# Kernel optimization log

Measured on AMD Instinct MI355X. Metric: run time of the kernel, lower is better.

## Reference

```python
import jax, jax.numpy as jnp
import numpy as np

EMBED_DIM = 2048
NUM_HEADS = 16
HEAD_DIM = EMBED_DIM // NUM_HEADS  # 128
D_K = 128
SCALE = 1.0 / float(np.sqrt(HEAD_DIM))
LAYER_DEPTH = 6 / 12  # amrpa_layer_idx / n_amrpa_layers
BATCH, SEQ = 2, 2048


def setup_inputs() -> dict:
    key = jax.random.key(0)
    ks = jax.random.split(key, 8)
    return {
        "hidden_states": jax.random.normal(ks[0], (BATCH, SEQ, EMBED_DIM), jnp.float32),
        "c_attn_w": jax.random.normal(ks[1], (EMBED_DIM, 3 * EMBED_DIM), jnp.float32) * 0.02,
        "c_attn_b": jax.random.normal(ks[2], (3 * EMBED_DIM,), jnp.float32) * 0.02,
        "c_proj_w": jax.random.normal(ks[3], (EMBED_DIM, EMBED_DIM), jnp.float32) * 0.02,
        "c_proj_b": jax.random.normal(ks[4], (EMBED_DIM,), jnp.float32) * 0.02,
        "cam_gate": jax.random.normal(ks[5], (D_K,), jnp.float32) * 0.1,
        "cam_w0": jax.random.normal(ks[6], (1,), jnp.float32),
        "cam_w1": jax.random.normal(ks[7], (1,), jnp.float32),
    }


def reference(hidden_states, c_attn_w, c_attn_b, c_proj_w, c_proj_b, cam_gate, cam_w0, cam_w1):
    # GPT2 Conv1D-style fused QKV projection: [B,S,3E]
    qkv = hidden_states @ c_attn_w + c_attn_b
    Q, K, V = jnp.split(qkv, 3, axis=2)  # each [B,S,E]
    # NOTE: faithful to source — attention over the FULL embed dim (no head split),
    # scaled by 1/sqrt(head_dim); causal mask is computed but never applied upstream.
    attn_scores = jnp.einsum('bse,bte->bst', Q, K) * SCALE  # [B,S,S]

    # CAM: sliced low-rank channels
    Q_cam, K_cam, V_cam = Q[:, :, :D_K], K[:, :, :D_K], V[:, :, :D_K]
    # base attention map computed under no_grad in the original
    base_A = jax.lax.stop_gradient(
        jax.nn.softmax(jnp.einsum('bsd,btd->bst', Q_cam, K_cam) * SCALE, axis=-1))
    layer_weight = jax.nn.sigmoid(cam_w0[0] + cam_w1[0] * LAYER_DEPTH)
    cam_ctx = jnp.einsum('bst,btd->bsd', base_A, V_cam)            # [B,S,d_k]
    cam_bias = jnp.einsum('bsd,btd->bst', jnp.tanh(cam_ctx * cam_gate), K_cam)
    cam_bias = cam_bias * (SCALE * layer_weight)                   # cam_mask is all-ones

    final_attn = jax.nn.softmax(attn_scores + cam_bias, axis=-1)
    context = jnp.einsum('bst,bte->bse', final_attn, V)            # [B,S,E]
    output = context @ c_proj_w + c_proj_b                         # resid_dropout is identity (eval)
    return output
```

## Files before the change

kernel.cpp:

```cpp
#include <hip/hip_runtime.h>
#include <hip/hip_bf16.h>

typedef unsigned short u16;
typedef __attribute__((ext_vector_type(8))) __bf16 bf16x8;
typedef __attribute__((ext_vector_type(4))) float f32x4;
typedef __attribute__((ext_vector_type(4))) unsigned short u16x4;

#define SCALE_QK 0.08838834764831845f

__device__ __forceinline__ u16 f2bf(float x) {
  union { float f; unsigned u; } v; v.f = x;
  unsigned r = v.u + 0x7fffu + ((v.u >> 16) & 1u);
  return (u16)(r >> 16);
}

__device__ __forceinline__ void gload_lds16(const u16* g, u16* l) {
  __builtin_amdgcn_global_load_lds(
      (const __attribute__((address_space(1))) unsigned*)g,
      (__attribute__((address_space(3))) unsigned*)l, 16, 0, 0);
}

#define CFENCE() asm volatile("" ::: "memory")

template<bool OUT_BF16, bool HAS_BIAS, bool TWO_SEG>
__global__ __launch_bounds__(512, 2)
void gemm256_8ph(const u16* __restrict__ A1, int lda1, long sA1,
                 const u16* __restrict__ B1, int ldb1, long sB1, int K1,
                 const u16* __restrict__ A2, int lda2, long sA2,
                 const u16* __restrict__ B2, int ldb2, long sB2, int K2,
                 void* __restrict__ Cv, int ldc, long sC,
                 float scale, const float* __restrict__ bias, int nbx)
{
  extern __shared__ u16 lds[];
  const int bz = blockIdx.z;

  const int nwg = gridDim.x;
  const int orig = blockIdx.x;
  const int q8 = nwg >> 3, r8 = nwg & 7;
  const int xcd = orig & 7, lp = orig >> 3;
  const int wg = (xcd < r8 ? xcd * (q8 + 1) : r8 * (q8 + 1) + (xcd - r8) * q8) + lp;
  const int bx = wg % nbx, by = wg / nbx;
  const long m0 = (long)by * 256, n0 = (long)bx * 256;

  const int tid = threadIdx.x;
  const int wid = tid >> 6, lane = tid & 63;
  const int wm = wid >> 2, wn = wid & 3;
  const int rl = lane & 15, g = lane >> 4;
  const int swk = ((g ^ ((rl >> 1) & 3)) << 3);

  int aoff[8], boff[4];
#pragma unroll
  for (int i = 0; i < 8; ++i)
    aoff[i] = (wm * 128 + i * 16 + rl) * 32 + swk;
#pragma unroll
  for (int j = 0; j < 4; ++j)
    boff[j] = 16384 + (wn * 64 + j * 16 + rl) * 32 + swk;

  const int Rl = tid >> 2;
  const int scol = (((tid & 3) ^ ((tid >> 3) & 3)) << 3);
  const int sdst = wid * 512;

  f32x4 acc[8][4];
#pragma unroll
  for (int i = 0; i < 8; ++i)
#pragma unroll
    for (int j = 0; j < 4; ++j) acc[i][j] = (f32x4){0.f, 0.f, 0.f, 0.f};

#define STAGE_A(KK, KB, BQ)                                                  \
  gload_lds16(rA0 + (KB) + (KK) * 32, (BQ) + (KK) * 8192 + sdst);            \
  gload_lds16(rA1 + (KB) + (KK) * 32, (BQ) + (KK) * 8192 + 4096 + sdst);
#define STAGE_B(KK, KB, BQ)                                                  \
  gload_lds16(rB0 + (KB) + (KK) * 32, (BQ) + 16384 + (KK) * 8192 + sdst);    \
  gload_lds16(rB1 + (KB) + (KK) * 32, (BQ) + 16384 + (KK) * 8192 + 4096 + sdst);
#define PHASE_MFMA(IH)                                                       \
  __builtin_amdgcn_s_setprio(1);                                             \
  _Pragma("unroll")                                                          \
  for (int i = 0; i < 4; ++i)                                                \
    _Pragma("unroll")                                                        \
    for (int j = 0; j < 4; ++j)                                              \
      acc[(IH) * 4 + i][j] = __builtin_amdgcn_mfma_f32_16x16x32_bf16(        \
          av[i], bv[j], acc[(IH) * 4 + i][j], 0, 0, 0);                      \
  __builtin_amdgcn_s_setprio(0);

  const int NSEG = TWO_SEG ? 2 : 1;
#pragma unroll 1
  for (int seg = 0; seg < NSEG; ++seg) {
    const u16* Ap = (seg == 0) ? (A1 + (long)bz * sA1) : (A2 + (long)bz * sA2);
    const u16* Bp = (seg == 0) ? (B1 + (long)bz * sB1) : (B2 + (long)bz * sB2);
    const int lda = (seg == 0) ? lda1 : lda2;
    const int ldb = (seg == 0) ? ldb1 : ldb2;
    const int K   = (seg == 0) ? K1 : K2;
    const int NT  = K >> 6;

    const u16* rA0 = Ap + (m0 + Rl) * (long)lda + scol;
    const u16* rA1 = Ap + (m0 + Rl + 128) * (long)lda + scol;
    const u16* rB0 = Bp + (n0 + Rl) * (long)ldb + scol;
    const u16* rB1 = Bp + (n0 + Rl + 128) * (long)ldb + scol;

    __builtin_amdgcn_s_barrier();
    CFENCE();
    STAGE_A(0, 0, lds);
    STAGE_B(0, 0, lds);
    STAGE_A(1, 0, lds);
    STAGE_B(1, 0, lds);
    CFENCE();

#pragma unroll 1
    for (int t = 0; t < NT; ++t) {
      const u16* bp = lds + (t & 1) * 32768;
      u16* bq = lds + ((t + 1) & 1) * 32768;
      const bool hn = (t + 1) < NT;
      const int kn = (t + 1) << 6;

      bf16x8 av[4], bv[4];

      asm volatile("s_waitcnt vmcnt(4)" ::: "memory");
      __builtin_amdgcn_s_barrier();
      CFENCE();
      if (hn) { STAGE_A(0, kn, bq); }
#pragma unroll
      for (int i = 0; i < 4; ++i) av[i] = *(const bf16x8*)(bp + aoff[i]);
#pragma unroll
      for (int j = 0; j < 4; ++j) bv[j] = *(const bf16x8*)(bp + boff[j]);
      PHASE_MFMA(0)
      CFENCE();

      if (hn) { STAGE_B(0, kn, bq); }
#pragma unroll
      for (int i = 0; i < 4; ++i) av[i] = *(const bf16x8*)(bp + aoff[4 + i]);
      PHASE_MFMA(1)
      CFENCE();

      if (hn) { asm volatile("s_waitcnt vmcnt(4)" ::: "memory"); }
      else    { asm volatile("s_waitcnt vmcnt(0)" ::: "memory"); }
      __builtin_amdgcn_s_barrier();
      CFENCE();
      if (hn) { STAGE_A(1, kn, bq); }
#pragma unroll
      for (int i = 0; i < 4; ++i) av[i] = *(const bf16x8*)(bp + 8192 + aoff[i]);
#pragma unroll
      for (int j = 0; j < 4; ++j) bv[j] = *(const bf16x8*)(bp + 8192 + boff[j]);
      PHASE_MFMA(0)
      CFENCE();

      if (hn) { STAGE_B(1, kn, bq); }
#pragma unroll
      for (int i = 0; i < 4; ++i) av[i] = *(const bf16x8*)(bp + 8192 + aoff[4 + i]);
      PHASE_MFMA(1)
      CFENCE();
    }
  }
#undef STAGE_A
#undef STAGE_B
#undef PHASE_MFMA

  const int r0 = (lane >> 4) << 2;
  const int cL = lane & 15;
#pragma unroll
  for (int i = 0; i < 8; ++i) {
#pragma unroll
    for (int j = 0; j < 4; ++j) {
      const long row = m0 + wm * 128 + i * 16 + r0;
      const long col = n0 + wn * 64 + j * 16 + cL;
      float bvs = 0.f;
      if (HAS_BIAS) bvs = bias[col];
      if (OUT_BF16) {
        u16* Cp = (u16*)Cv + (long)bz * sC;
#pragma unroll
        for (int r = 0; r < 4; ++r)
          Cp[(row + r) * ldc + col] = f2bf(acc[i][j][r] * scale + bvs);
      } else {
        float* Cp = (float*)Cv + (long)bz * sC;
#pragma unroll
        for (int r = 0; r < 4; ++r)
          Cp[(row + r) * ldc + col] = acc[i][j][r] * scale + bvs;
      }
    }
  }
}

template<bool OUT_BF16, bool HAS_BIAS>
__global__ __launch_bounds__(256)
void gemm_bt(const u16* __restrict__ A, int lda, long sA,
             const u16* __restrict__ B, int ldb, long sB,
             void* __restrict__ Cv, int ldc, long sC,
             int K, float scale, const float* __restrict__ bias)
{
  __shared__ u16 As[128 * 64];
  __shared__ u16 Bs[128 * 64];
  const int bz   = blockIdx.z;
  const u16* Ap  = A + (long)bz * sA;
  const u16* Bp  = B + (long)bz * sB;
  const int tid  = threadIdx.x;
  const int wid  = tid >> 6;
  const int lane = tid & 63;
  const long m0  = (long)blockIdx.y * 128;
  const long n0  = (long)blockIdx.x * 128;
  const int lrow = lane >> 3;
  const int lk   = (lane & 7) << 3;
  const int wr   = wid >> 1, wc = wid & 1;

  f32x4 acc[4][4];
#pragma unroll
  for (int i = 0; i < 4; ++i)
#pragma unroll
    for (int j = 0; j < 4; ++j) acc[i][j] = (f32x4){0.f, 0.f, 0.f, 0.f};

  for (int k0 = 0; k0 < K; k0 += 64) {
#pragma unroll
    for (int c4 = 0; c4 < 4; ++c4) {
      const int chunk = (wid << 2) + c4;
      gload_lds16(Ap + (m0 + (chunk << 3) + lrow) * lda + k0 + lk, &As[chunk << 9]);
      gload_lds16(Bp + (n0 + (chunk << 3) + lrow) * ldb + k0 + lk, &Bs[chunk << 9]);
    }
    __syncthreads();
#pragma unroll
    for (int kk = 0; kk < 2; ++kk) {
      bf16x8 af[4], bfr[4];
      const int kof   = (kk << 5) + ((lane >> 4) << 3);
      const int rbase = lane & 15;
#pragma unroll
      for (int i = 0; i < 4; ++i)
        af[i] = *(const bf16x8*)&As[(((wr << 6) + (i << 4) + rbase) << 6) + kof];
#pragma unroll
      for (int j = 0; j < 4; ++j)
        bfr[j] = *(const bf16x8*)&Bs[(((wc << 6) + (j << 4) + rbase) << 6) + kof];
#pragma unroll
      for (int i = 0; i < 4; ++i)
#pragma unroll
        for (int j = 0; j < 4; ++j)
          acc[i][j] = __builtin_amdgcn_mfma_f32_16x16x32_bf16(af[i], bfr[j], acc[i][j], 0, 0, 0);
    }
    __syncthreads();
  }

  const int r0 = (lane >> 4) << 2;
  const int cL = lane & 15;
#pragma unroll
  for (int i = 0; i < 4; ++i) {
#pragma unroll
    for (int j = 0; j < 4; ++j) {
      const long row = m0 + (wr << 6) + (i << 4) + r0;
      const long col = n0 + (wc << 6) + (j << 4) + cL;
      float bv = 0.f;
      if (HAS_BIAS) bv = bias[col];
      if (OUT_BF16) {
        u16* Cp = (u16*)Cv + (long)bz * sC;
#pragma unroll
        for (int r = 0; r < 4; ++r)
          Cp[(row + r) * ldc + col] = f2bf(acc[i][j][r] * scale + bv);
      } else {
        float* Cp = (float*)Cv + (long)bz * sC;
#pragma unroll
        for (int r = 0; r < 4; ++r)
          Cp[(row + r) * ldc + col] = acc[i][j][r] * scale + bv;
      }
    }
  }
}

__global__ __launch_bounds__(256)
void gemm_bt_splitk(const u16* __restrict__ A, int lda, long sA,
                    const u16* __restrict__ B, int ldb, long sB,
                    float* __restrict__ C, int ldc, long sC,
                    int Kslice, float scale)
{
  __shared__ u16 As[128 * 64];
  __shared__ u16 Bs[128 * 64];
  const int ks = blockIdx.z & 7;
  const int bz = blockIdx.z >> 3;
  const u16* Ap  = A + (long)bz * sA + ks * Kslice;
  const u16* Bp  = B + (long)bz * sB + ks * Kslice;
  const int tid  = threadIdx.x;
  const int wid  = tid >> 6;
  const int lane = tid & 63;
  const long m0  = (long)blockIdx.y * 128;
  const long n0  = (long)blockIdx.x * 128;
  const int lrow = lane >> 3;
  const int lk   = (lane & 7) << 3;
  const int wr   = wid >> 1, wc = wid & 1;

  f32x4 acc[4][4];
#pragma unroll
  for (int i = 0; i < 4; ++i)
#pragma unroll
    for (int j = 0; j < 4; ++j) acc[i][j] = (f32x4){0.f, 0.f, 0.f, 0.f};

  for (int k0 = 0; k0 < Kslice; k0 += 64) {
#pragma unroll
    for (int c4 = 0; c4 < 4; ++c4) {
      const int chunk = (wid << 2) + c4;
      gload_lds16(Ap + (m0 + (chunk << 3) + lrow) * lda + k0 + lk, &As[chunk << 9]);
      gload_lds16(Bp + (n0 + (chunk << 3) + lrow) * ldb + k0 + lk, &Bs[chunk << 9]);
    }
    __syncthreads();
#pragma unroll
    for (int kk = 0; kk < 2; ++kk) {
      bf16x8 af[4], bfr[4];
      const int kof   = (kk << 5) + ((lane >> 4) << 3);
      const int rbase = lane & 15;
#pragma unroll
      for (int i = 0; i < 4; ++i)
        af[i] = *(const bf16x8*)&As[(((wr << 6) + (i << 4) + rbase) << 6) + kof];
#pragma unroll
      for (int j = 0; j < 4; ++j)
        bfr[j] = *(const bf16x8*)&Bs[(((wc << 6) + (j << 4) + rbase) << 6) + kof];
#pragma unroll
      for (int i = 0; i < 4; ++i)
#pragma unroll
        for (int j = 0; j < 4; ++j)
          acc[i][j] = __builtin_amdgcn_mfma_f32_16x16x32_bf16(af[i], bfr[j], acc[i][j], 0, 0, 0);
    }
    __syncthreads();
  }

  const int r0 = (lane >> 4) << 2;
  const int cL = lane & 15;
  float* Cp = C + (long)bz * sC;
#pragma unroll
  for (int i = 0; i < 4; ++i) {
#pragma unroll
    for (int j = 0; j < 4; ++j) {
      const long row = m0 + (wr << 6) + (i << 4) + r0;
      const long col = n0 + (wc << 6) + (j << 4) + cL;
#pragma unroll
      for (int r = 0; r < 4; ++r)
        atomicAdd(&Cp[(row + r) * ldc + col], acc[i][j][r] * scale);
    }
  }
}

__global__ __launch_bounds__(256)
void softmax_rows2048(const float* __restrict__ src, u16* __restrict__ dst) {
  const long row = blockIdx.x;
  const float4* s = (const float4*)(src + row * 2048);
  const int tid = threadIdx.x;
  float4 a = s[tid * 2], b = s[tid * 2 + 1];
  float m = fmaxf(fmaxf(fmaxf(a.x, a.y), fmaxf(a.z, a.w)),
                  fmaxf(fmaxf(b.x, b.y), fmaxf(b.z, b.w)));
#pragma unroll
  for (int o = 32; o > 0; o >>= 1) m = fmaxf(m, __shfl_xor(m, o));
  __shared__ float redm[4];
  __shared__ float reds[4];
  if ((tid & 63) == 0) redm[tid >> 6] = m;
  __syncthreads();
  m = fmaxf(fmaxf(redm[0], redm[1]), fmaxf(redm[2], redm[3]));
  float e[8];
  e[0] = __expf(a.x - m); e[1] = __expf(a.y - m); e[2] = __expf(a.z - m); e[3] = __expf(a.w - m);
  e[4] = __expf(b.x - m); e[5] = __expf(b.y - m); e[6] = __expf(b.z - m); e[7] = __expf(b.w - m);
  float sum = e[0] + e[1] + e[2] + e[3] + e[4] + e[5] + e[6] + e[7];
#pragma unroll
  for (int o = 32; o > 0; o >>= 1) sum += __shfl_xor(sum, o);
  if ((tid & 63) == 0) reds[tid >> 6] = sum;
  __syncthreads();
  sum = reds[0] + reds[1] + reds[2] + reds[3];
  const float inv = 1.f / sum;
  u16x4 o1 = { f2bf(e[0] * inv), f2bf(e[1] * inv), f2bf(e[2] * inv), f2bf(e[3] * inv) };
  u16x4 o2 = { f2bf(e[4] * inv), f2bf(e[5] * inv), f2bf(e[6] * inv), f2bf(e[7] * inv) };
  u16x4* d = (u16x4*)(dst + row * 2048);
  d[tid * 2]     = o1;
  d[tid * 2 + 1] = o2;
}

__global__ void transpose_f32_to_bf16(const float* __restrict__ src, u16* __restrict__ dst,
                                      int R, int C) {
  __shared__ float t[32][33];
  const int c0 = blockIdx.x * 32, r0 = blockIdx.y * 32;
  const int tx = threadIdx.x, ty = threadIdx.y;
#pragma unroll
  for (int i = 0; i < 4; ++i)
    t[ty + i * 8][tx] = src[(long)(r0 + ty + i * 8) * C + c0 + tx];
  __syncthreads();
#pragma unroll
  for (int i = 0; i < 4; ++i)
    dst[(long)(c0 + ty + i * 8) * R + r0 + tx] = f2bf(t[tx][ty + i * 8]);
}

__global__ void transpose_bf16_batched(const u16* __restrict__ src, int ss, long sbat,
                                       u16* __restrict__ dst, int ds, long dbat) {
  __shared__ u16 t[32][33];
  const u16* s = src + (long)blockIdx.z * sbat;
  u16* d = dst + (long)blockIdx.z * dbat;
  const int c0 = blockIdx.x * 32, r0 = blockIdx.y * 32;
  const int tx = threadIdx.x, ty = threadIdx.y;
#pragma unroll
  for (int i = 0; i < 4; ++i)
    t[ty + i * 8][tx] = s[(long)(r0 + ty + i * 8) * ss + c0 + tx];
  __syncthreads();
#pragma unroll
  for (int i = 0; i < 4; ++i)
    d[(long)(c0 + ty + i * 8) * ds + r0 + tx] = t[tx][ty + i * 8];
}

__global__ __launch_bounds__(256)
void convert_f32_to_bf16(const float* __restrict__ src, u16* __restrict__ dst, long n4) {
  long i = (long)blockIdx.x * 256 + threadIdx.x;
  if (i < n4) {
    float4 v = ((const float4*)src)[i];
    *(u16x4*)(dst + i * 4) = (u16x4){ f2bf(v.x), f2bf(v.y), f2bf(v.z), f2bf(v.w) };
  }
}

__global__ __launch_bounds__(256)
void cam_tanh_kernel(const float* __restrict__ ctx, const float* __restrict__ gate,
                     const float* __restrict__ lw, u16* __restrict__ out, int n) {
  int i = blockIdx.x * 256 + threadIdx.x;
  if (i < n) {
    int d = i & 127;
    out[i] = f2bf(tanhf(ctx[i] * gate[d]) * lw[0]);
  }
}

__global__ __launch_bounds__(256)
void zero_f32(float* __restrict__ p, int n) {
  int i = blockIdx.x * 256 + threadIdx.x;
  if (i < n) p[i] = 0.f;
}

__global__ void calc_lw_kernel(const float* w0, const float* w1, float* lw) {
  *lw = 1.f / (1.f + __expf(-(w0[0] + 0.5f * w1[0])));
}

extern "C" void kernel_launch(void* const* d_in, const int* in_sizes, int n_in,
                              void* d_out, int out_size, void* d_ws, size_t ws_size,
                              hipStream_t stream) {
  const float* hs       = (const float*)d_in[0];
  const float* c_attn_w = (const float*)d_in[1];
  const float* c_attn_b = (const float*)d_in[2];
  const float* c_proj_w = (const float*)d_in[3];
  const float* c_proj_b = (const float*)d_in[4];
  const float* cam_gate = (const float*)d_in[5];
  const float* cam_w0   = (const float*)d_in[6];
  const float* cam_w1   = (const float*)d_in[7];
  float* out = (float*)d_out;

  char* w = (char*)d_ws;
  float* lw      = (float*)(w + 0);
  u16*   hs_b    = (u16*)(w + 256);
  u16*   waT_b   = (u16*)(w + 256 + 16777216UL);
  u16*   wpT_b   = (u16*)(w + 256 + 41943040UL);
  u16*   qkv_b   = (u16*)(w + 256 + 50331648UL);
  u16*   vT_b    = (u16*)(w + 256 + 100663296UL);
  float* scoresF = (float*)(w + 256 + 117440512UL);
  float* camS    = (float*)(w + 256 + 150994944UL);
  float* ctxF    = (float*)(w + 256 + 184549376UL);
  u16*   camT_b  = (u16*)(w + 256 + 186646528UL);
  u16* baseA_b = hs_b;
  u16* P_b     = (u16*)camS;
  u16* ctxE_b  = (u16*)scoresF;

  dim3 b256(256);

  hipFuncSetAttribute((const void*)gemm256_8ph<true,  true,  false>,
                      hipFuncAttributeMaxDynamicSharedMemorySize, 131072);
  hipFuncSetAttribute((const void*)gemm256_8ph<false, false, true>,
                      hipFuncAttributeMaxDynamicSharedMemorySize, 131072);
  hipFuncSetAttribute((const void*)gemm256_8ph<true,  false, false>,
                      hipFuncAttributeMaxDynamicSharedMemorySize, 131072);
  hipFuncSetAttribute((const void*)gemm256_8ph<false, true,  false>,
                      hipFuncAttributeMaxDynamicSharedMemorySize, 131072);

  calc_lw_kernel<<<dim3(1), dim3(1), 0, stream>>>(cam_w0, cam_w1, lw);
  convert_f32_to_bf16<<<dim3(8192), b256, 0, stream>>>(hs, hs_b, 2097152L);
  transpose_f32_to_bf16<<<dim3(192, 64), dim3(32, 8), 0, stream>>>(c_attn_w, waT_b, 2048, 6144);
  transpose_f32_to_bf16<<<dim3(64, 64), dim3(32, 8), 0, stream>>>(c_proj_w, wpT_b, 2048, 2048);

  gemm256_8ph<true, true, false><<<dim3(384, 1, 1), dim3(512), 131072, stream>>>(
      hs_b, 2048, 0L, waT_b, 2048, 0L, 2048,
      nullptr, 0, 0L, nullptr, 0, 0L, 0,
      qkv_b, 6144, 0L, 1.f, c_attn_b, 24);

  transpose_bf16_batched<<<dim3(64, 64, 2), dim3(32, 8), 0, stream>>>(
      qkv_b + 4096, 6144, 2048L * 6144, vT_b, 2048, 2048L * 2048);

  gemm_bt<false, false><<<dim3(16, 16, 2), b256, 0, stream>>>(
      qkv_b, 6144, 2048L * 6144, qkv_b + 2048, 6144, 2048L * 6144,
      camS, 2048, 2048L * 2048, 128, SCALE_QK, nullptr);

  softmax_rows2048<<<dim3(4096), b256, 0, stream>>>(camS, baseA_b);

  zero_f32<<<dim3(2048), b256, 0, stream>>>(ctxF, 524288);
  gemm_bt_splitk<<<dim3(1, 16, 16), b256, 0, stream>>>(
      baseA_b, 2048, 2048L * 2048, vT_b, 2048, 2048L * 2048,
      ctxF, 128, 2048L * 128, 256, 1.f);

  cam_tanh_kernel<<<dim3(2048), b256, 0, stream>>>(ctxF, cam_gate, lw, camT_b, 524288);

  gemm256_8ph<false, false, true><<<dim3(64, 1, 2), dim3(512), 131072, stream>>>(
      qkv_b, 6144, 2048L * 6144, qkv_b + 2048, 6144, 2048L * 6144, 2048,
      camT_b, 128, 2048L * 128, qkv_b + 2048, 6144, 2048L * 6144, 128,
      scoresF, 2048, 2048L * 2048, SCALE_QK, nullptr, 8);

  softmax_rows2048<<<dim3(4096), b256, 0, stream>>>(scoresF, P_b);

  gemm256_8ph<true, false, false><<<dim3(64, 1, 2), dim3(512), 131072, stream>>>(
      P_b, 2048, 2048L * 2048, vT_b, 2048, 2048L * 2048, 2048,
      nullptr, 0, 0L, nullptr, 0, 0L, 0,
      ctxE_b, 2048, 2048L * 2048, 1.f, nullptr, 8);

  gemm256_8ph<false, true, false><<<dim3(128, 1, 1), dim3(512), 131072, stream>>>(
      ctxE_b, 2048, 0L, wpT_b, 2048, 0L, 2048,
      nullptr, 0, 0L, nullptr, 0, 0L, 0,
      out, 2048, 0L, 1.f, c_proj_b, 8);
}
```

Before: 392.4 us.

## Deepen GEMM LDS pipeline to 4 stages and add 256x128 tile variant

The 256x256 GEMM is rebuilt around a 4-slot LDS ring of 32-wide K halves. It keeps three stages in flight, with explicit vmcnt waits and sched barriers around the MFMA phases instead of the old double buffer. A new 256x128 tile kernel with the same deeper prefetch replaces the 256x256 kernel for the score, PV and output-projection GEMMs. This doubles their grid sizes so more of the GPU's compute units are filled. The cost is more B-operand reloads per output and more barriers per K step.

```diff
diff --git a/kernel.cpp b/kernel.cpp
--- a/kernel.cpp
+++ b/kernel.cpp
@@ -21,146 +21,234 @@
 }
 
 #define CFENCE() asm volatile("" ::: "memory")
-
-template<bool OUT_BF16, bool HAS_BIAS, bool TWO_SEG>
+#define WAITV(N) asm volatile("s_waitcnt vmcnt(" #N ")" ::: "memory")
+
+#define MM_PROLOG()                                                      \
+  CFENCE(); __builtin_amdgcn_s_barrier();                                \
+  asm volatile("s_waitcnt lgkmcnt(0)" ::: "memory");                     \
+  __builtin_amdgcn_sched_barrier(0);                                     \
+  __builtin_amdgcn_s_setprio(1);
+#define MM_EPILOG()                                                      \
+  __builtin_amdgcn_s_setprio(0);                                         \
+  CFENCE(); __builtin_amdgcn_s_barrier(); CFENCE();
+
+template<bool OUT_BF16, bool HAS_BIAS>
 __global__ __launch_bounds__(512, 2)
-void gemm256_8ph(const u16* __restrict__ A1, int lda1, long sA1,
-                 const u16* __restrict__ B1, int ldb1, long sB1, int K1,
-                 const u16* __restrict__ A2, int lda2, long sA2,
-                 const u16* __restrict__ B2, int ldb2, long sB2, int K2,
-                 void* __restrict__ Cv, int ldc, long sC,
-                 float scale, const float* __restrict__ bias, int nbx)
+void g256(const u16* __restrict__ A, int lda, long sA,
+          const u16* __restrict__ B, int ldb, long sB,
+          void* __restrict__ Cv, int ldc, long sC,
+          int K, float scale, const float* __restrict__ bias, int nbx)
 {
   extern __shared__ u16 lds[];
   const int bz = blockIdx.z;
-
-  const int nwg = gridDim.x;
-  const int orig = blockIdx.x;
+  const int nwg = gridDim.x, orig = blockIdx.x;
   const int q8 = nwg >> 3, r8 = nwg & 7;
   const int xcd = orig & 7, lp = orig >> 3;
   const int wg = (xcd < r8 ? xcd * (q8 + 1) : r8 * (q8 + 1) + (xcd - r8) * q8) + lp;
   const int bx = wg % nbx, by = wg / nbx;
   const long m0 = (long)by * 256, n0 = (long)bx * 256;
 
-  const int tid = threadIdx.x;
-  const int wid = tid >> 6, lane = tid & 63;
+  const int tid = threadIdx.x, wid = tid >> 6, lane = tid & 63;
   const int wm = wid >> 2, wn = wid & 3;
   const int rl = lane & 15, g = lane >> 4;
-  const int swk = ((g ^ ((rl >> 1) & 3)) << 3);
+  const int sw = ((g ^ ((rl >> 1) & 3)) << 3);
 
   int aoff[8], boff[4];
 #pragma unroll
+  for (int i = 0; i < 8; ++i) aoff[i] = (wm * 128 + i * 16 + rl) * 32 + sw;
+#pragma unroll
+  for (int j = 0; j < 4; ++j) boff[j] = (wn * 64 + j * 16 + rl) * 32 + sw;
+
+  const u16* Ab = A + (long)bz * sA + m0 * lda;
+  const u16* Bb = B + (long)bz * sB + n0 * ldb;
+  const int srow = tid >> 2;
+  const int scolX = (((tid & 3) ^ ((srow >> 1) & 3)) << 3);
+
+#define ST_A(H_) {                                                       \
+    const u16* s_ = Ab + (long)srow * lda + (H_) * 32 + scolX;           \
+    u16* d_ = lds + (((H_) & 3) * 8192) + tid * 8;                       \
+    gload_lds16(s_, d_); gload_lds16(s_ + (long)128 * lda, d_ + 4096); }
+#define ST_B(H_) {                                                       \
+    const u16* s_ = Bb + (long)srow * ldb + (H_) * 32 + scolX;           \
+    u16* d_ = lds + 32768 + (((H_) & 3) * 8192) + tid * 8;               \
+    gload_lds16(s_, d_); gload_lds16(s_ + (long)128 * ldb, d_ + 4096); }
+#define RDA(H_, IH) { const u16* aS_ = lds + ((H_) & 3) * 8192;          \
+    _Pragma("unroll") for (int i = 0; i < 4; ++i)                        \
+      av[i] = *(const bf16x8*)(aS_ + aoff[(IH) * 4 + i]); }
+#define RDB(H_) { const u16* bS_ = lds + 32768 + ((H_) & 3) * 8192;      \
+    _Pragma("unroll") for (int j = 0; j < 4; ++j)                        \
+      bv[j] = *(const bf16x8*)(bS_ + boff[j]); }
+#define MFMA16(IH)                                                       \
+  MM_PROLOG();                                                           \
+  _Pragma("unroll") for (int i = 0; i < 4; ++i)                          \
+    _Pragma("unroll") for (int j = 0; j < 4; ++j)                        \
+      acc[(IH) * 4 + i][j] = __builtin_amdgcn_mfma_f32_16x16x32_bf16(    \
+          av[i], bv[j], acc[(IH) * 4 + i][j], 0, 0, 0);                  \
+  MM_EPILOG();
+
+  f32x4 acc[8][4];
+#pragma unroll
   for (int i = 0; i < 8; ++i)
-    aoff[i] = (wm * 128 + i * 16 + rl) * 32 + swk;
-#pragma unroll
-  for (int j = 0; j < 4; ++j)
-    boff[j] = 16384 + (wn * 64 + j * 16 + rl) * 32 + swk;
-
-  const int Rl = tid >> 2;
-  const int scol = (((tid & 3) ^ ((tid >> 3) & 3)) << 3);
-  const int sdst = wid * 512;
-
-  f32x4 acc[8][4];
-#pragma unroll
-  for (int i = 0; i < 8; ++i)
 #pragma unroll
     for (int j = 0; j < 4; ++j) acc[i][j] = (f32x4){0.f, 0.f, 0.f, 0.f};
 
-#define STAGE_A(KK, KB, BQ)                                                  \
-  gload_lds16(rA0 + (KB) + (KK) * 32, (BQ) + (KK) * 8192 + sdst);            \
-  gload_lds16(rA1 + (KB) + (KK) * 32, (BQ) + (KK) * 8192 + 4096 + sdst);
-#define STAGE_B(KK, KB, BQ)                                                  \
-  gload_lds16(rB0 + (KB) + (KK) * 32, (BQ) + 16384 + (KK) * 8192 + sdst);    \
-  gload_lds16(rB1 + (KB) + (KK) * 32, (BQ) + 16384 + (KK) * 8192 + 4096 + sdst);
-#define PHASE_MFMA(IH)                                                       \
-  __builtin_amdgcn_s_setprio(1);                                             \
-  _Pragma("unroll")                                                          \
-  for (int i = 0; i < 4; ++i)                                                \
-    _Pragma("unroll")                                                        \
-    for (int j = 0; j < 4; ++j)                                              \
-      acc[(IH) * 4 + i][j] = __builtin_amdgcn_mfma_f32_16x16x32_bf16(        \
-          av[i], bv[j], acc[(IH) * 4 + i][j], 0, 0, 0);                      \
-  __builtin_amdgcn_s_setprio(0);
+  const int NT = K >> 6;
+
+  ST_A(0); ST_B(0); ST_A(1); ST_B(1); ST_A(2); ST_B(2);
+  WAITV(8);
+  CFENCE(); __builtin_amdgcn_s_barrier(); CFENCE();
+
+#pragma unroll 1
+  for (int t = 0; t < NT - 2; ++t) {
+    const int h0 = 2 * t, h1 = 2 * t + 1;
+    bf16x8 av[4], bv[4];
+    RDA(h0, 0); RDB(h0); ST_A(h1 + 2); MFMA16(0);
+    RDA(h0, 1); ST_B(h1 + 2); WAITV(8); MFMA16(1);
+    RDA(h1, 0); RDB(h1); ST_A(h1 + 3); MFMA16(0);
+    RDA(h1, 1); ST_B(h1 + 3); WAITV(8); MFMA16(1);
+  }
+  {
+    const int h0 = 2 * NT - 4, h1 = 2 * NT - 3;
+    bf16x8 av[4], bv[4];
+    RDA(h0, 0); RDB(h0); ST_A(2 * NT - 1); MFMA16(0);
+    RDA(h0, 1); ST_B(2 * NT - 1); WAITV(8); MFMA16(1);
+    RDA(h1, 0); RDB(h1); MFMA16(0);
+    RDA(h1, 1); WAITV(4); MFMA16(1);
+  }
+  {
+    const int h0 = 2 * NT - 2, h1 = 2 * NT - 1;
+    bf16x8 av[4], bv[4];
+    RDA(h0, 0); RDB(h0); MFMA16(0);
+    RDA(h0, 1); WAITV(0); MFMA16(1);
+    RDA(h1, 0); RDB(h1); MFMA16(0);
+    RDA(h1, 1); MFMA16(1);
+  }
+#undef ST_A
+#undef ST_B
+#undef RDA
+#undef RDB
+#undef MFMA16
+
+  const int r0 = (lane >> 4) << 2;
+  const int cL = lane & 15;
+#pragma unroll
+  for (int i = 0; i < 8; ++i) {
+#pragma unroll
+    for (int j = 0; j < 4; ++j) {
+      const long row = m0 + wm * 128 + i * 16 + r0;
+      const long col = n0 + wn * 64 + j * 16 + cL;
+      float bvs = 0.f;
+      if (HAS_BIAS) bvs = bias[col];
+      if (OUT_BF16) {
+        u16* Cp = (u16*)Cv + (long)bz * sC;
+#pragma unroll
+        for (int r = 0; r < 4; ++r)
+          Cp[(row + r) * ldc + col] = f2bf(acc[i][j][r] * scale + bvs);
+      } else {
+        float* Cp = (float*)Cv + (long)bz * sC;
+#pragma unroll
+        for (int r = 0; r < 4; ++r)
+          Cp[(row + r) * ldc + col] = acc[i][j][r] * scale + bvs;
+      }
+    }
+  }
+}
+
+template<bool OUT_BF16, bool HAS_BIAS, bool TWO_SEG>
+__global__ __launch_bounds__(512, 2)
+void g128(const u16* __restrict__ A1, int lda1, long sA1,
+          const u16* __restrict__ B1, int ldb1, long sB1, int K1,
+          const u16* __restrict__ A2, int lda2, long sA2,
+          const u16* __restrict__ B2, int ldb2, long sB2, int K2,
+          void* __restrict__ Cv, int ldc, long sC,
+          float scale, const float* __restrict__ bias, int nbx)
+{
+  extern __shared__ u16 lds[];
+  const int bz = blockIdx.z;
+  const int nwg = gridDim.x, orig = blockIdx.x;
+  const int q8 = nwg >> 3, r8 = nwg & 7;
+  const int xcd = orig & 7, lp = orig >> 3;
+  const int wg = (xcd < r8 ? xcd * (q8 + 1) : r8 * (q8 + 1) + (xcd - r8) * q8) + lp;
+  const int bx = wg % nbx, by = wg / nbx;
+  const long m0 = (long)by * 256, n0 = (long)bx * 128;
+
+  const int tid = threadIdx.x, wid = tid >> 6, lane = tid & 63;
+  const int wm = wid >> 1, wn = wid & 1;
+  const int rl = lane & 15, g = lane >> 4;
+  const int sw = ((g ^ ((rl >> 1) & 3)) << 3);
+
+  int aoff[4], boff[4];
+#pragma unroll
+  for (int i = 0; i < 4; ++i) aoff[i] = (wm * 64 + i * 16 + rl) * 32 + sw;
+#pragma unroll
+  for (int j = 0; j < 4; ++j) boff[j] = (wn * 64 + j * 16 + rl) * 32 + sw;
+
+  const int srow = tid >> 2;
+  const int scolX = (((tid & 3) ^ ((srow >> 1) & 3)) << 3);
+
+  f32x4 acc[4][4];
+#pragma unroll
+  for (int i = 0; i < 4; ++i)
+#pragma unroll
+    for (int j = 0; j < 4; ++j) acc[i][j] = (f32x4){0.f, 0.f, 0.f, 0.f};
+
+#define STG128(H_) {                                                     \
+    const u16* sa_ = Ab + (long)srow * lda + (H_) * 32 + scolX;          \
+    u16* da_ = lds + (((H_) & 3) * 8192) + tid * 8;                      \
+    gload_lds16(sa_, da_); gload_lds16(sa_ + (long)128 * lda, da_ + 4096); \
+    gload_lds16(Bb + (long)srow * ldb + (H_) * 32 + scolX,               \
+                lds + 32768 + (((H_) & 3) * 4096) + tid * 8); }
+#define RD128(H_) {                                                      \
+    const u16* aS_ = lds + ((H_) & 3) * 8192;                            \
+    const u16* bS_ = lds + 32768 + ((H_) & 3) * 4096;                    \
+    _Pragma("unroll") for (int i = 0; i < 4; ++i)                        \
+      av[i] = *(const bf16x8*)(aS_ + aoff[i]);                           \
+    _Pragma("unroll") for (int j = 0; j < 4; ++j)                        \
+      bv[j] = *(const bf16x8*)(bS_ + boff[j]); }
+#define MM128()                                                          \
+  MM_PROLOG();                                                           \
+  _Pragma("unroll") for (int i = 0; i < 4; ++i)                          \
+    _Pragma("unroll") for (int j = 0; j < 4; ++j)                        \
+      acc[i][j] = __builtin_amdgcn_mfma_f32_16x16x32_bf16(               \
+          av[i], bv[j], acc[i][j], 0, 0, 0);                             \
+  MM_EPILOG();
 
   const int NSEG = TWO_SEG ? 2 : 1;
 #pragma unroll 1
   for (int seg = 0; seg < NSEG; ++seg) {
-    const u16* Ap = (seg == 0) ? (A1 + (long)bz * sA1) : (A2 + (long)bz * sA2);
-    const u16* Bp = (seg == 0) ? (B1 + (long)bz * sB1) : (B2 + (long)bz * sB2);
+    const u16* Ab = ((seg == 0) ? A1 + (long)bz * sA1 : A2 + (long)bz * sA2);
+    const u16* Bb = ((seg == 0) ? B1 + (long)bz * sB1 : B2 + (long)bz * sB2);
     const int lda = (seg == 0) ? lda1 : lda2;
     const int ldb = (seg == 0) ? ldb1 : ldb2;
     const int K   = (seg == 0) ? K1 : K2;
-    const int NT  = K >> 6;
-
-    const u16* rA0 = Ap + (m0 + Rl) * (long)lda + scol;
-    const u16* rA1 = Ap + (m0 + Rl + 128) * (long)lda + scol;
-    const u16* rB0 = Bp + (n0 + Rl) * (long)ldb + scol;
-    const u16* rB1 = Bp + (n0 + Rl + 128) * (long)ldb + scol;
-
-    __builtin_amdgcn_s_barrier();
-    CFENCE();
-    STAGE_A(0, 0, lds);
-    STAGE_B(0, 0, lds);
-    STAGE_A(1, 0, lds);
-    STAGE_B(1, 0, lds);
-    CFENCE();
+    Ab += m0 * lda;
+    Bb += n0 * ldb;
+    const int H = K >> 5;
+
+    bf16x8 av[4], bv[4];
+    STG128(0); STG128(1); STG128(2);
+    WAITV(6);
+    CFENCE(); __builtin_amdgcn_s_barrier(); CFENCE();
 
 #pragma unroll 1
-    for (int t = 0; t < NT; ++t) {
-      const u16* bp = lds + (t & 1) * 32768;
-      u16* bq = lds + ((t + 1) & 1) * 32768;
-      const bool hn = (t + 1) < NT;
-      const int kn = (t + 1) << 6;
-
-      bf16x8 av[4], bv[4];
-
-      asm volatile("s_waitcnt vmcnt(4)" ::: "memory");
-      __builtin_amdgcn_s_barrier();
-      CFENCE();
-      if (hn) { STAGE_A(0, kn, bq); }
-#pragma unroll
-      for (int i = 0; i < 4; ++i) av[i] = *(const bf16x8*)(bp + aoff[i]);
-#pragma unroll
-      for (int j = 0; j < 4; ++j) bv[j] = *(const bf16x8*)(bp + boff[j]);
-      PHASE_MFMA(0)
-      CFENCE();
-
-      if (hn) { STAGE_B(0, kn, bq); }
-#pragma unroll
-      for (int i = 0; i < 4; ++i) av[i] = *(const bf16x8*)(bp + aoff[4 + i]);
-      PHASE_MFMA(1)
-      CFENCE();
-
-      if (hn) { asm volatile("s_waitcnt vmcnt(4)" ::: "memory"); }
-      else    { asm volatile("s_waitcnt vmcnt(0)" ::: "memory"); }
-      __builtin_amdgcn_s_barrier();
-      CFENCE();
-      if (hn) { STAGE_A(1, kn, bq); }
-#pragma unroll
-      for (int i = 0; i < 4; ++i) av[i] = *(const bf16x8*)(bp + 8192 + aoff[i]);
-#pragma unroll
-      for (int j = 0; j < 4; ++j) bv[j] = *(const bf16x8*)(bp + 8192 + boff[j]);
-      PHASE_MFMA(0)
-      CFENCE();
-
-      if (hn) { STAGE_B(1, kn, bq); }
-#pragma unroll
-      for (int i = 0; i < 4; ++i) av[i] = *(const bf16x8*)(bp + 8192 + aoff[4 + i]);
-      PHASE_MFMA(1)
-      CFENCE();
-    }
-  }
-#undef STAGE_A
-#undef STAGE_B
-#undef PHASE_MFMA
+    for (int h = 0; h < H - 3; ++h) {
+      RD128(h); STG128(h + 3); WAITV(6); MM128();
+    }
+    RD128(H - 3); WAITV(3); MM128();
+    RD128(H - 2); WAITV(0); MM128();
+    RD128(H - 1); MM128();
+  }
+#undef STG128
+#undef RD128
+#undef MM128
 
   const int r0 = (lane >> 4) << 2;
   const int cL = lane & 15;
 #pragma unroll
-  for (int i = 0; i < 8; ++i) {
+  for (int i = 0; i < 4; ++i) {
 #pragma unroll
     for (int j = 0; j < 4; ++j) {
-      const long row = m0 + wm * 128 + i * 16 + r0;
+      const long row = m0 + wm * 64 + i * 16 + r0;
       const long col = n0 + wn * 64 + j * 16 + cL;
       float bvs = 0.f;
       if (HAS_BIAS) bvs = bias[col];
@@ -451,24 +539,23 @@
 
   dim3 b256(256);
 
-  hipFuncSetAttribute((const void*)gemm256_8ph<true,  true,  false>,
+  hipFuncSetAttribute((const void*)g256<true, true>,
                       hipFuncAttributeMaxDynamicSharedMemorySize, 131072);
-  hipFuncSetAttribute((const void*)gemm256_8ph<false, false, true>,
-                      hipFuncAttributeMaxDynamicSharedMemorySize, 131072);
-  hipFuncSetAttribute((const void*)gemm256_8ph<true,  false, false>,
-                      hipFuncAttributeMaxDynamicSharedMemorySize, 131072);
-  hipFuncSetAttribute((const void*)gemm256_8ph<false, true,  false>,
-                      hipFuncAttributeMaxDynamicSharedMemorySize, 131072);
+  hipFuncSetAttribute((const void*)g128<false, false, true>,
+                      hipFuncAttributeMaxDynamicSharedMemorySize, 98304);
+  hipFuncSetAttribute((const void*)g128<true, false, false>,
+                      hipFuncAttributeMaxDynamicSharedMemorySize, 98304);
+  hipFuncSetAttribute((const void*)g128<false, true, false>,
+                      hipFuncAttributeMaxDynamicSharedMemorySize, 98304);
 
   calc_lw_kernel<<<dim3(1), dim3(1), 0, stream>>>(cam_w0, cam_w1, lw);
   convert_f32_to_bf16<<<dim3(8192), b256, 0, stream>>>(hs, hs_b, 2097152L);
   transpose_f32_to_bf16<<<dim3(192, 64), dim3(32, 8), 0, stream>>>(c_attn_w, waT_b, 2048, 6144);
   transpose_f32_to_bf16<<<dim3(64, 64), dim3(32, 8), 0, stream>>>(c_proj_w, wpT_b, 2048, 2048);
 
-  gemm256_8ph<true, true, false><<<dim3(384, 1, 1), dim3(512), 131072, stream>>>(
-      hs_b, 2048, 0L, waT_b, 2048, 0L, 2048,
-      nullptr, 0, 0L, nullptr, 0, 0L, 0,
-      qkv_b, 6144, 0L, 1.f, c_attn_b, 24);
+  g256<true, true><<<dim3(384, 1, 1), dim3(512), 131072, stream>>>(
+      hs_b, 2048, 0L, waT_b, 2048, 0L,
+      qkv_b, 6144, 0L, 2048, 1.f, c_attn_b, 24);
 
   transpose_bf16_batched<<<dim3(64, 64, 2), dim3(32, 8), 0, stream>>>(
       qkv_b + 4096, 6144, 2048L * 6144, vT_b, 2048, 2048L * 2048);
@@ -486,20 +573,20 @@
 
   cam_tanh_kernel<<<dim3(2048), b256, 0, stream>>>(ctxF, cam_gate, lw, camT_b, 524288);
 
-  gemm256_8ph<false, false, true><<<dim3(64, 1, 2), dim3(512), 131072, stream>>>(
+  g128<false, false, true><<<dim3(128, 1, 2), dim3(512), 98304, stream>>>(
       qkv_b, 6144, 2048L * 6144, qkv_b + 2048, 6144, 2048L * 6144, 2048,
       camT_b, 128, 2048L * 128, qkv_b + 2048, 6144, 2048L * 6144, 128,
-      scoresF, 2048, 2048L * 2048, SCALE_QK, nullptr, 8);
+      scoresF, 2048, 2048L * 2048, SCALE_QK, nullptr, 16);
 
   softmax_rows2048<<<dim3(4096), b256, 0, stream>>>(scoresF, P_b);
 
-  gemm256_8ph<true, false, false><<<dim3(64, 1, 2), dim3(512), 131072, stream>>>(
+  g128<true, false, false><<<dim3(128, 1, 2), dim3(512), 98304, stream>>>(
       P_b, 2048, 2048L * 2048, vT_b, 2048, 2048L * 2048, 2048,
       nullptr, 0, 0L, nullptr, 0, 0L, 0,
-      ctxE_b, 2048, 2048L * 2048, 1.f, nullptr, 8);
-
-  gemm256_8ph<false, true, false><<<dim3(128, 1, 1), dim3(512), 131072, stream>>>(
+      ctxE_b, 2048, 2048L * 2048, 1.f, nullptr, 16);
+
+  g128<false, true, false><<<dim3(256, 1, 1), dim3(512), 98304, stream>>>(
       ctxE_b, 2048, 0L, wpT_b, 2048, 0L, 2048,
       nullptr, 0, 0L, nullptr, 0, 0L, 0,
-      out, 2048, 0L, 1.f, c_proj_b, 8);
-}
+      out, 2048, 0L, 1.f, c_proj_b, 16);
+}
```

Result: faster. 349.9 us (median of 2 runs) (-10.8%).

## Replace 256x256 GEMM with 256x128 tile and 4-stage LDS pipeline

Applied to the files above, without the earlier changes.

The main GEMM kernel changes from 256x256 output tiles with a two-buffer, K=64 schedule to 256x128 tiles with a four-stage ring of K=32 LDS slices. Register fragments are double-buffered so the LDS reads for the next slice are issued after the current MFMAs. Grids double to keep the same coverage, and LDS per block drops to 96KB. This aims to put more workgroups on the GPU and hide more global-load latency, at the cost of lower arithmetic intensity per tile and more redundant global traffic.

```diff
diff --git a/kernel.cpp b/kernel.cpp
--- a/kernel.cpp
+++ b/kernel.cpp
@@ -21,146 +21,116 @@
 }
 
 #define CFENCE() asm volatile("" ::: "memory")
+#define WAITV(N) asm volatile("s_waitcnt vmcnt(" #N ")" ::: "memory")
 
 template<bool OUT_BF16, bool HAS_BIAS, bool TWO_SEG>
 __global__ __launch_bounds__(512, 2)
-void gemm256_8ph(const u16* __restrict__ A1, int lda1, long sA1,
-                 const u16* __restrict__ B1, int ldb1, long sB1, int K1,
-                 const u16* __restrict__ A2, int lda2, long sA2,
-                 const u16* __restrict__ B2, int ldb2, long sB2, int K2,
-                 void* __restrict__ Cv, int ldc, long sC,
-                 float scale, const float* __restrict__ bias, int nbx)
+void g128p(const u16* __restrict__ A1, int lda1, long sA1,
+           const u16* __restrict__ B1, int ldb1, long sB1, int K1,
+           const u16* __restrict__ A2, int lda2, long sA2,
+           const u16* __restrict__ B2, int ldb2, long sB2, int K2,
+           void* __restrict__ Cv, int ldc, long sC,
+           float scale, const float* __restrict__ bias, int nbx)
 {
   extern __shared__ u16 lds[];
   const int bz = blockIdx.z;
-
-  const int nwg = gridDim.x;
-  const int orig = blockIdx.x;
+  const int nwg = gridDim.x, orig = blockIdx.x;
   const int q8 = nwg >> 3, r8 = nwg & 7;
   const int xcd = orig & 7, lp = orig >> 3;
   const int wg = (xcd < r8 ? xcd * (q8 + 1) : r8 * (q8 + 1) + (xcd - r8) * q8) + lp;
   const int bx = wg % nbx, by = wg / nbx;
-  const long m0 = (long)by * 256, n0 = (long)bx * 256;
-
-  const int tid = threadIdx.x;
-  const int wid = tid >> 6, lane = tid & 63;
-  const int wm = wid >> 2, wn = wid & 3;
+  const long m0 = (long)by * 256, n0 = (long)bx * 128;
+
+  const int tid = threadIdx.x, wid = tid >> 6, lane = tid & 63;
+  const int wm = wid >> 1, wn = wid & 1;
   const int rl = lane & 15, g = lane >> 4;
-  const int swk = ((g ^ ((rl >> 1) & 3)) << 3);
-
-  int aoff[8], boff[4];
-#pragma unroll
-  for (int i = 0; i < 8; ++i)
-    aoff[i] = (wm * 128 + i * 16 + rl) * 32 + swk;
-#pragma unroll
-  for (int j = 0; j < 4; ++j)
-    boff[j] = 16384 + (wn * 64 + j * 16 + rl) * 32 + swk;
-
-  const int Rl = tid >> 2;
-  const int scol = (((tid & 3) ^ ((tid >> 3) & 3)) << 3);
-  const int sdst = wid * 512;
-
-  f32x4 acc[8][4];
-#pragma unroll
-  for (int i = 0; i < 8; ++i)
+  const int sw = ((g ^ ((rl >> 1) & 3)) << 3);
+
+  int aoff[4], boff[4];
+#pragma unroll
+  for (int i = 0; i < 4; ++i) aoff[i] = (wm * 64 + i * 16 + rl) * 32 + sw;
+#pragma unroll
+  for (int j = 0; j < 4; ++j) boff[j] = (wn * 64 + j * 16 + rl) * 32 + sw;
+
+  const int srow = tid >> 2;
+  const int scolX = (((tid & 3) ^ ((srow >> 1) & 3)) << 3);
+
+  f32x4 acc[4][4];
+#pragma unroll
+  for (int i = 0; i < 4; ++i)
 #pragma unroll
     for (int j = 0; j < 4; ++j) acc[i][j] = (f32x4){0.f, 0.f, 0.f, 0.f};
 
-#define STAGE_A(KK, KB, BQ)                                                  \
-  gload_lds16(rA0 + (KB) + (KK) * 32, (BQ) + (KK) * 8192 + sdst);            \
-  gload_lds16(rA1 + (KB) + (KK) * 32, (BQ) + (KK) * 8192 + 4096 + sdst);
-#define STAGE_B(KK, KB, BQ)                                                  \
-  gload_lds16(rB0 + (KB) + (KK) * 32, (BQ) + 16384 + (KK) * 8192 + sdst);    \
-  gload_lds16(rB1 + (KB) + (KK) * 32, (BQ) + 16384 + (KK) * 8192 + 4096 + sdst);
-#define PHASE_MFMA(IH)                                                       \
-  __builtin_amdgcn_s_setprio(1);                                             \
-  _Pragma("unroll")                                                          \
-  for (int i = 0; i < 4; ++i)                                                \
-    _Pragma("unroll")                                                        \
-    for (int j = 0; j < 4; ++j)                                              \
-      acc[(IH) * 4 + i][j] = __builtin_amdgcn_mfma_f32_16x16x32_bf16(        \
-          av[i], bv[j], acc[(IH) * 4 + i][j], 0, 0, 0);                      \
-  __builtin_amdgcn_s_setprio(0);
+  bf16x8 avA[4], bvA[4], avB[4], bvB[4];
+
+#define STG(H_) {                                                        \
+    const int h_ = (H_);                                                 \
+    const u16* sa_ = Ab + (long)srow * lda + h_ * 32 + scolX;            \
+    u16* da_ = lds + ((h_ & 3) * 8192) + tid * 8;                        \
+    gload_lds16(sa_, da_);                                               \
+    gload_lds16(sa_ + (long)128 * lda, da_ + 4096);                      \
+    gload_lds16(Bb + (long)srow * ldb + h_ * 32 + scolX,                 \
+                lds + 32768 + ((h_ & 3) * 4096) + tid * 8); }
+#define RD(H_, AV, BV) {                                                 \
+    const u16* aS_ = lds + (((H_) & 3) * 8192);                          \
+    const u16* bS_ = lds + 32768 + (((H_) & 3) * 4096);                  \
+    _Pragma("unroll") for (int i_ = 0; i_ < 4; ++i_)                     \
+      AV[i_] = *(const bf16x8*)(aS_ + aoff[i_]);                         \
+    _Pragma("unroll") for (int j_ = 0; j_ < 4; ++j_)                     \
+      BV[j_] = *(const bf16x8*)(bS_ + boff[j_]); }
+#define BODY(K_, CAV, CBV, NAV, NBV, W_STMT, DO_RD, DO_ST)               \
+    W_STMT;                                                              \
+    CFENCE(); __builtin_amdgcn_s_barrier(); CFENCE();                    \
+    asm volatile("s_waitcnt lgkmcnt(0)" ::: "memory");                   \
+    __builtin_amdgcn_sched_barrier(0);                                   \
+    __builtin_amdgcn_s_setprio(1);                                       \
+    _Pragma("unroll") for (int i_ = 0; i_ < 4; ++i_)                     \
+      _Pragma("unroll") for (int j_ = 0; j_ < 4; ++j_)                   \
+        acc[i_][j_] = __builtin_amdgcn_mfma_f32_16x16x32_bf16(           \
+            CAV[i_], CBV[j_], acc[i_][j_], 0, 0, 0);                     \
+    __builtin_amdgcn_s_setprio(0);                                       \
+    if (DO_RD) { RD((K_) + 1, NAV, NBV); }                               \
+    if (DO_ST) { STG((K_) + 4); }                                        \
+    CFENCE();
 
   const int NSEG = TWO_SEG ? 2 : 1;
 #pragma unroll 1
   for (int seg = 0; seg < NSEG; ++seg) {
-    const u16* Ap = (seg == 0) ? (A1 + (long)bz * sA1) : (A2 + (long)bz * sA2);
-    const u16* Bp = (seg == 0) ? (B1 + (long)bz * sB1) : (B2 + (long)bz * sB2);
     const int lda = (seg == 0) ? lda1 : lda2;
     const int ldb = (seg == 0) ? ldb1 : ldb2;
     const int K   = (seg == 0) ? K1 : K2;
-    const int NT  = K >> 6;
-
-    const u16* rA0 = Ap + (m0 + Rl) * (long)lda + scol;
-    const u16* rA1 = Ap + (m0 + Rl + 128) * (long)lda + scol;
-    const u16* rB0 = Bp + (n0 + Rl) * (long)ldb + scol;
-    const u16* rB1 = Bp + (n0 + Rl + 128) * (long)ldb + scol;
-
-    __builtin_amdgcn_s_barrier();
+    const u16* Ab = ((seg == 0) ? A1 + (long)bz * sA1 : A2 + (long)bz * sA2) + m0 * (long)lda;
+    const u16* Bb = ((seg == 0) ? B1 + (long)bz * sB1 : B2 + (long)bz * sB2) + n0 * (long)ldb;
+    const int H = K >> 5;
+
+    STG(0); STG(1); STG(2);
+    WAITV(6);
+    CFENCE(); __builtin_amdgcn_s_barrier(); CFENCE();
+    RD(0, avA, bvA);
+    STG(3);
     CFENCE();
-    STAGE_A(0, 0, lds);
-    STAGE_B(0, 0, lds);
-    STAGE_A(1, 0, lds);
-    STAGE_B(1, 0, lds);
-    CFENCE();
 
 #pragma unroll 1
-    for (int t = 0; t < NT; ++t) {
-      const u16* bp = lds + (t & 1) * 32768;
-      u16* bq = lds + ((t + 1) & 1) * 32768;
-      const bool hn = (t + 1) < NT;
-      const int kn = (t + 1) << 6;
-
-      bf16x8 av[4], bv[4];
-
-      asm volatile("s_waitcnt vmcnt(4)" ::: "memory");
-      __builtin_amdgcn_s_barrier();
-      CFENCE();
-      if (hn) { STAGE_A(0, kn, bq); }
-#pragma unroll
-      for (int i = 0; i < 4; ++i) av[i] = *(const bf16x8*)(bp + aoff[i]);
-#pragma unroll
-      for (int j = 0; j < 4; ++j) bv[j] = *(const bf16x8*)(bp + boff[j]);
-      PHASE_MFMA(0)
-      CFENCE();
-
-      if (hn) { STAGE_B(0, kn, bq); }
-#pragma unroll
-      for (int i = 0; i < 4; ++i) av[i] = *(const bf16x8*)(bp + aoff[4 + i]);
-      PHASE_MFMA(1)
-      CFENCE();
-
-      if (hn) { asm volatile("s_waitcnt vmcnt(4)" ::: "memory"); }
-      else    { asm volatile("s_waitcnt vmcnt(0)" ::: "memory"); }
-      __builtin_amdgcn_s_barrier();
-      CFENCE();
-      if (hn) { STAGE_A(1, kn, bq); }
-#pragma unroll
-      for (int i = 0; i < 4; ++i) av[i] = *(const bf16x8*)(bp + 8192 + aoff[i]);
-#pragma unroll
-      for (int j = 0; j < 4; ++j) bv[j] = *(const bf16x8*)(bp + 8192 + boff[j]);
-      PHASE_MFMA(0)
-      CFENCE();
-
-      if (hn) { STAGE_B(1, kn, bq); }
-#pragma unroll
-      for (int i = 0; i < 4; ++i) av[i] = *(const bf16x8*)(bp + 8192 + aoff[4 + i]);
-      PHASE_MFMA(1)
-      CFENCE();
-    }
-  }
-#undef STAGE_A
-#undef STAGE_B
-#undef PHASE_MFMA
+    for (int k = 0; k + 5 < H; k += 2) {
+      BODY(k,     avA, bvA, avB, bvB, WAITV(6), true, true);
+      BODY(k + 1, avB, bvB, avA, bvA, WAITV(6), true, true);
+    }
+    BODY(H - 4, avA, bvA, avB, bvB, WAITV(6), true,  false);
+    BODY(H - 3, avB, bvB, avA, bvA, WAITV(3), true,  false);
+    BODY(H - 2, avA, bvA, avB, bvB, WAITV(0), true,  false);
+    BODY(H - 1, avB, bvB, avA, bvA, (void)0,  false, false);
+  }
+#undef STG
+#undef RD
+#undef BODY
 
   const int r0 = (lane >> 4) << 2;
   const int cL = lane & 15;
 #pragma unroll
-  for (int i = 0; i < 8; ++i) {
+  for (int i = 0; i < 4; ++i) {
 #pragma unroll
     for (int j = 0; j < 4; ++j) {
-      const long row = m0 + wm * 128 + i * 16 + r0;
+      const long row = m0 + wm * 64 + i * 16 + r0;
       const long col = n0 + wn * 64 + j * 16 + cL;
       float bvs = 0.f;
       if (HAS_BIAS) bvs = bias[col];
@@ -451,24 +421,24 @@
 
   dim3 b256(256);
 
-  hipFuncSetAttribute((const void*)gemm256_8ph<true,  true,  false>,
-                      hipFuncAttributeMaxDynamicSharedMemorySize, 131072);
-  hipFuncSetAttribute((const void*)gemm256_8ph<false, false, true>,
-                      hipFuncAttributeMaxDynamicSharedMemorySize, 131072);
-  hipFuncSetAttribute((const void*)gemm256_8ph<true,  false, false>,
-                      hipFuncAttributeMaxDynamicSharedMemorySize, 131072);
-  hipFuncSetAttribute((const void*)gemm256_8ph<false, true,  false>,
-                      hipFuncAttributeMaxDynamicSharedMemorySize, 131072);
+  hipFuncSetAttribute((const void*)g128p<true, true, false>,
+                      hipFuncAttributeMaxDynamicSharedMemorySize, 98304);
+  hipFuncSetAttribute((const void*)g128p<false, false, true>,
+                      hipFuncAttributeMaxDynamicSharedMemorySize, 98304);
+  hipFuncSetAttribute((const void*)g128p<true, false, false>,
+                      hipFuncAttributeMaxDynamicSharedMemorySize, 98304);
+  hipFuncSetAttribute((const void*)g128p<false, true, false>,
+                      hipFuncAttributeMaxDynamicSharedMemorySize, 98304);
 
   calc_lw_kernel<<<dim3(1), dim3(1), 0, stream>>>(cam_w0, cam_w1, lw);
   convert_f32_to_bf16<<<dim3(8192), b256, 0, stream>>>(hs, hs_b, 2097152L);
   transpose_f32_to_bf16<<<dim3(192, 64), dim3(32, 8), 0, stream>>>(c_attn_w, waT_b, 2048, 6144);
   transpose_f32_to_bf16<<<dim3(64, 64), dim3(32, 8), 0, stream>>>(c_proj_w, wpT_b, 2048, 2048);
 
-  gemm256_8ph<true, true, false><<<dim3(384, 1, 1), dim3(512), 131072, stream>>>(
+  g128p<true, true, false><<<dim3(768, 1, 1), dim3(512), 98304, stream>>>(
       hs_b, 2048, 0L, waT_b, 2048, 0L, 2048,
       nullptr, 0, 0L, nullptr, 0, 0L, 0,
-      qkv_b, 6144, 0L, 1.f, c_attn_b, 24);
+      qkv_b, 6144, 0L, 1.f, c_attn_b, 48);
 
   transpose_bf16_batched<<<dim3(64, 64, 2), dim3(32, 8), 0, stream>>>(
       qkv_b + 4096, 6144, 2048L * 6144, vT_b, 2048, 2048L * 2048);
@@ -486,20 +456,20 @@
 
   cam_tanh_kernel<<<dim3(2048), b256, 0, stream>>>(ctxF, cam_gate, lw, camT_b, 524288);
 
-  gemm256_8ph<false, false, true><<<dim3(64, 1, 2), dim3(512), 131072, stream>>>(
+  g128p<false, false, true><<<dim3(128, 1, 2), dim3(512), 98304, stream>>>(
       qkv_b, 6144, 2048L * 6144, qkv_b + 2048, 6144, 2048L * 6144, 2048,
       camT_b, 128, 2048L * 128, qkv_b + 2048, 6144, 2048L * 6144, 128,
-      scoresF, 2048, 2048L * 2048, SCALE_QK, nullptr, 8);
+      scoresF, 2048, 2048L * 2048, SCALE_QK, nullptr, 16);
 
   softmax_rows2048<<<dim3(4096), b256, 0, stream>>>(scoresF, P_b);
 
-  gemm256_8ph<true, false, false><<<dim3(64, 1, 2), dim3(512), 131072, stream>>>(
+  g128p<true, false, false><<<dim3(128, 1, 2), dim3(512), 98304, stream>>>(
       P_b, 2048, 2048L * 2048, vT_b, 2048, 2048L * 2048, 2048,
       nullptr, 0, 0L, nullptr, 0, 0L, 0,
-      ctxE_b, 2048, 2048L * 2048, 1.f, nullptr, 8);
-
-  gemm256_8ph<false, true, false><<<dim3(128, 1, 1), dim3(512), 131072, stream>>>(
+      ctxE_b, 2048, 2048L * 2048, 1.f, nullptr, 16);
+
+  g128p<false, true, false><<<dim3(256, 1, 1), dim3(512), 98304, stream>>>(
       ctxE_b, 2048, 0L, wpT_b, 2048, 0L, 2048,
       nullptr, 0, 0L, nullptr, 0, 0L, 0,
-      out, 2048, 0L, 1.f, c_proj_b, 8);
-}
+      out, 2048, 0L, 1.f, c_proj_b, 16);
+}
```

Measured after the change: 348.0 us. -11.3%, faster.
